# Kernel tuning notes

Hardware: AMD Instinct MI355X
Metric: run time of the kernel (lower is better)

## Reference

```python
import jax, jax.numpy as jnp
import numpy as np

B, S, D = 2, 4096, 2048
HQ, HK, HV = 32, 8, 8
H = max(HQ, HK, HV)
DK, DV = 64, 64
OUT = 2048
CHUNK = 64  # chunked-recurrent block size


def setup_inputs() -> dict:
    key = jax.random.key(0)
    k1, k2, k3 = jax.random.split(key, 3)
    x = jax.random.normal(k1, (B, S, D), dtype=jnp.float32)
    input_state = jnp.zeros((B, H * DK * DV), dtype=jnp.float32)
    qkv = HQ * DK + HK * DK + HV * DV  # 3072
    # Linear weights stored as [in, out]; equals torch weight.T so y = x @ W
    W_in = jax.random.normal(k2, (D, qkv), dtype=jnp.float32) * (D ** -0.5)
    W_out = jax.random.normal(k3, (H * DV, OUT), dtype=jnp.float32) * ((H * DV) ** -0.5)
    return {"x": x, "input_state": input_state, "W_in": W_in, "W_out": W_out}


def _linear_attention(q, k, v, S0):
    # q,k,v: [B,S,H,d]; S0: [B,H,DK,DV]
    nc = S // CHUNK
    # move chunk axis to front for lax.scan: [nc, B, CHUNK, H, d]
    qc = jnp.moveaxis(q.reshape(B, nc, CHUNK, H, DK), 1, 0)
    kc = jnp.moveaxis(k.reshape(B, nc, CHUNK, H, DK), 1, 0)
    vc = jnp.moveaxis(v.reshape(B, nc, CHUNK, H, DV), 1, 0)
    mask = jnp.tril(jnp.ones((CHUNK, CHUNK), dtype=bool))  # causal within chunk

    def step(Sstate, blk):
        qb, kb, vb = blk  # [B,C,H,d]
        A = jnp.einsum('bihd,bjhd->bhij', qb, kb)
        A = jnp.where(mask, A, jnp.zeros((), A.dtype))
        o = jnp.einsum('bhij,bjhd->bihd', A, vb) \
            + jnp.einsum('bihd,bhde->bihe', qb, Sstate)
        Sstate = Sstate + jnp.einsum('bjhd,bjhe->bhde', kb, vb)
        return Sstate, o

    Sf, o = jax.lax.scan(step, S0, (qc, kc, vc))
    o = jnp.moveaxis(o, 0, 1).reshape(B, S, H, DV)
    return o, Sf


def reference(x, input_state, W_in, W_out):
    proj = x @ W_in  # [B,S,3072]
    q, k, v = jnp.split(proj, [HQ * DK, HQ * DK + HK * DK], axis=-1)
    q = q.reshape(B, S, HQ, DK)
    k = k.reshape(B, S, HK, DK)
    v = v.reshape(B, S, HV, DV)
    # GQA: repeat kv heads up to num_heads = max(...)
    k = jnp.repeat(k, H // HK, axis=2)
    v = jnp.repeat(v, H // HV, axis=2)
    S0 = input_state.reshape(B, H, DK, DV)
    o, Sf = _linear_attention(q, k, v, S0)
    out = o.reshape(B, S, H * DV) @ W_out
    return out, Sf.reshape(B, H, DK * DV)
```

## Files before the change

### kernel.cpp

```cpp
#include <hip/hip_runtime.h>

typedef __bf16 bf16_t;
typedef __bf16 bf16x8 __attribute__((ext_vector_type(8)));
typedef __bf16 bf16x4 __attribute__((ext_vector_type(4)));
typedef float  f32x4  __attribute__((ext_vector_type(4)));

#define MFMA16(a,b,c) __builtin_amdgcn_mfma_f32_16x16x32_bf16((a),(b),(c),0,0,0)

__device__ __forceinline__ void gl_lds16(const void* g, void* l) {
    __builtin_amdgcn_global_load_lds(
        (__attribute__((address_space(1))) void*)(g),
        (__attribute__((address_space(3))) void*)(l),
        16, 0, 0);
}

static constexpr int S_TOT   = 8192;
static constexpr int D_IN    = 2048;
static constexpr int QKV     = 3072;
static constexpr int OUT_D   = 2048;
static constexpr int NCHUNK  = 64;
static constexpr int ZSTR    = 88;

__global__ __launch_bounds__(256)
void prep(const float* __restrict__ x, bf16_t* __restrict__ xb,
          const float* __restrict__ W_in, bf16_t* __restrict__ WinT,
          const float* __restrict__ W_out, bf16_t* __restrict__ WoutT) {
    __shared__ float tile[64][65];
    const int bid = blockIdx.x;
    const int t   = threadIdx.x;
    if (bid < 16384) {
        int i = bid * 256 + t;
        f32x4 v = ((const f32x4*)x)[i];
        bf16x4 o;
        o[0] = (bf16_t)v[0]; o[1] = (bf16_t)v[1]; o[2] = (bf16_t)v[2]; o[3] = (bf16_t)v[3];
        ((bf16x4*)xb)[i] = o;
        return;
    }
    const float* in; bf16_t* out; int R, C, bx, by;
    int tb = bid - 16384;
    if (tb < 1536) { in = W_in;  out = WinT;  R = 2048; C = 3072; bx = tb % 48; by = tb / 48; }
    else { tb -= 1536; in = W_out; out = WoutT; R = 2048; C = 2048; bx = tb % 32; by = tb / 32; }
    const int r0 = by * 64, c0 = bx * 64;
#pragma unroll
    for (int p = 0; p < 4; p++) {
        int row = p * 16 + (t >> 4);
        int col = (t & 15) * 4;
        f32x4 v = *(const f32x4*)&in[(size_t)(r0 + row) * C + c0 + col];
        tile[row][col + 0] = v[0]; tile[row][col + 1] = v[1];
        tile[row][col + 2] = v[2]; tile[row][col + 3] = v[3];
    }
    __syncthreads();
#pragma unroll
    for (int p = 0; p < 4; p++) {
        int oc  = p * 16 + (t >> 4);
        int orr = (t & 15) * 4;
        bf16x4 v;
        v[0] = (bf16_t)tile[orr + 0][oc]; v[1] = (bf16_t)tile[orr + 1][oc];
        v[2] = (bf16_t)tile[orr + 2][oc]; v[3] = (bf16_t)tile[orr + 3][oc];
        *(bf16x4*)&out[(size_t)(c0 + oc) * R + r0 + orr] = v;
    }
}

template<int OUT_BF16>
__global__ __launch_bounds__(256, 4)
void gemm_bt(const bf16_t* __restrict__ A, const bf16_t* __restrict__ Bt,
             void* __restrict__ Cout, int M, int N, int K) {
    __shared__ alignas(16) bf16_t lA[128 * 64];
    __shared__ alignas(16) bf16_t lB[128 * 64];
    const int tid = threadIdx.x;
    const int m0 = blockIdx.y * 128;
    const int n0 = blockIdx.x * 128;
    const int w = tid >> 6, lane = tid & 63;
    const int wr = (w >> 1) * 64, wc = (w & 1) * 64;
    const int l15 = lane & 15, q = lane >> 4, q4 = q * 4;
    const int trow = tid >> 3;
    const int tcc  = (tid & 7) ^ (trow & 7);
    const bf16_t* Ag = A + (size_t)(m0 + trow) * K + tcc * 8;
    const bf16_t* Bg = Bt + (size_t)(n0 + trow) * K + tcc * 8;
    bf16_t* lA_t = lA + tid * 8;
    bf16_t* lB_t = lB + tid * 8;
    const size_t rs = (size_t)32 * K;
    const int cc0 = (q)     ^ (l15 & 7);
    const int cc1 = (4 + q) ^ (l15 & 7);
    f32x4 acc[4][4] = {};
    for (int k0 = 0; k0 < K; k0 += 64) {
#pragma unroll
        for (int j = 0; j < 4; j++) {
            gl_lds16(Ag + k0 + j * rs, lA_t + j * 2048);
            gl_lds16(Bg + k0 + j * rs, lB_t + j * 2048);
        }
        __syncthreads();
#pragma unroll
        for (int ksub = 0; ksub < 2; ksub++) {
            const int cc = ksub ? cc1 : cc0;
            bf16x8 bfr[4];
#pragma unroll
            for (int nj = 0; nj < 4; nj++)
                bfr[nj] = *(const bf16x8*)&lB[(wc + nj * 16 + l15) * 64 + cc * 8];
#pragma unroll
            for (int mi = 0; mi < 4; mi++) {
                bf16x8 afr = *(const bf16x8*)&lA[(wr + mi * 16 + l15) * 64 + cc * 8];
#pragma unroll
                for (int nj = 0; nj < 4; nj++)
                    acc[mi][nj] = MFMA16(afr, bfr[nj], acc[mi][nj]);
            }
        }
        __syncthreads();
    }
    if (OUT_BF16) {
        bf16_t* C = (bf16_t*)Cout;
#pragma unroll
        for (int mi = 0; mi < 4; mi++)
#pragma unroll
            for (int nj = 0; nj < 4; nj++)
#pragma unroll
                for (int r = 0; r < 4; r++)
                    C[(size_t)(m0 + wr + mi * 16 + q4 + r) * N + n0 + wc + nj * 16 + l15] =
                        (bf16_t)acc[mi][nj][r];
    } else {
        float* C = (float*)Cout;
#pragma unroll
        for (int mi = 0; mi < 4; mi++)
#pragma unroll
            for (int nj = 0; nj < 4; nj++)
#pragma unroll
                for (int r = 0; r < 4; r++)
                    C[(size_t)(m0 + wr + mi * 16 + q4 + r) * N + n0 + wc + nj * 16 + l15] =
                        acc[mi][nj][r];
    }
}

__global__ __launch_bounds__(64)
void kv_fused(const bf16_t* __restrict__ proj, bf16_t* __restrict__ vT_g,
              float* __restrict__ Zc) {
    const int idx = blockIdx.x;
    const int c = idx & 63, hk = (idx >> 6) & 7, b = idx >> 9;
    const int tokBase = b * 4096 + c * 64;
    __shared__ float tk[64][65];
    __shared__ float tv[64][65];
    const int lane = threadIdx.x;
    const bf16_t* kg = proj + (size_t)tokBase * QKV + 2048 + hk * 64;
    const bf16_t* vg = proj + (size_t)tokBase * QKV + 2560 + hk * 64;
#pragma unroll
    for (int p = 0; p < 8; p++) {
        int tok = p * 8 + (lane >> 3);
        int d0  = (lane & 7) * 8;
        bf16x8 kv = *(const bf16x8*)&kg[(size_t)tok * QKV + d0];
        bf16x8 vv = *(const bf16x8*)&vg[(size_t)tok * QKV + d0];
#pragma unroll
        for (int e = 0; e < 8; e++) {
            tk[tok][d0 + e] = (float)kv[e];
            tv[tok][d0 + e] = (float)vv[e];
        }
    }
    __syncthreads();
#pragma unroll
    for (int p = 0; p < 8; p++) {
        int dv = p * 8 + (lane >> 3);
        int t0 = (lane & 7) * 8;
        bf16x8 o;
#pragma unroll
        for (int e = 0; e < 8; e++) o[e] = (bf16_t)tv[t0 + e][dv];
        *(bf16x8*)&vT_g[(size_t)idx * 4096 + dv * 64 + t0] = o;
    }
    const int l15 = lane & 15, q8 = (lane >> 4) * 8, q4 = (lane >> 4) * 4;
    f32x4 acc[4][4] = {};
#pragma unroll
    for (int ks = 0; ks < 2; ks++) {
        bf16x8 af[4], bf_[4];
#pragma unroll
        for (int mi = 0; mi < 4; mi++)
#pragma unroll
            for (int e = 0; e < 8; e++) af[mi][e] = (bf16_t)tv[ks * 32 + q8 + e][mi * 16 + l15];
#pragma unroll
        for (int nj = 0; nj < 4; nj++)
#pragma unroll
            for (int e = 0; e < 8; e++) bf_[nj][e] = (bf16_t)tk[ks * 32 + q8 + e][nj * 16 + l15];
#pragma unroll
        for (int mi = 0; mi < 4; mi++)
#pragma unroll
            for (int nj = 0; nj < 4; nj++)
                acc[mi][nj] = MFMA16(af[mi], bf_[nj], acc[mi][nj]);
    }
    float* zout = Zc + (size_t)idx * 4096;
#pragma unroll
    for (int mi = 0; mi < 4; mi++)
#pragma unroll
        for (int nj = 0; nj < 4; nj++)
#pragma unroll
            for (int r = 0; r < 4; r++)
                zout[(mi * 16 + q4 + r) * 64 + nj * 16 + l15] = acc[mi][nj][r];
}

__global__ __launch_bounds__(256)
void prefix_state(const float* __restrict__ Zc, const float* __restrict__ S0,
                  bf16_t* __restrict__ Zp, float* __restrict__ SfOut) {
    const int slice = blockIdx.x & 15;
    const int bh = blockIdx.x >> 4;
    const int h = bh & 31, b = bh >> 5;
    const int hk = h >> 2;
    const int e = slice * 256 + threadIdx.x;
    const int dv = e >> 6, dk = e & 63;
    float acc = S0[(size_t)b * 131072 + h * 4096 + dk * 64 + dv];
    const float* zc = Zc + ((size_t)(b * 8 + hk) * 64) * 4096 + e;
    bf16_t* zp = Zp + ((size_t)(b * 32 + h) * 64) * 4096 + e;
#pragma unroll 4
    for (int c = 0; c < NCHUNK; c++) {
        zp[(size_t)c * 4096] = (bf16_t)acc;
        acc += zc[(size_t)c * 4096];
    }
    SfOut[(size_t)b * 131072 + h * 4096 + dk * 64 + dv] = acc;
}

__global__ __launch_bounds__(256)
void attn_chunk(const bf16_t* __restrict__ proj, const bf16_t* __restrict__ vT_g,
                const bf16_t* __restrict__ Zp, bf16_t* __restrict__ O) {
    const int idx = blockIdx.x;
    const int hk = idx & 7, c = (idx >> 3) & 63, b = idx >> 9;
    const int g = threadIdx.x >> 6, lane = threadIdx.x & 63;
    const int h = hk * 4 + g;
    const int tokBase = b * 4096 + c * 64;
    __shared__ alignas(16) bf16_t zs_all[4][64 * ZSTR];
    bf16_t* zs = zs_all[g];
    const int l15 = lane & 15, q8 = (lane >> 4) * 8, q4 = (lane >> 4) * 4;
    const bf16_t* qrow  = proj + (size_t)tokBase * QKV + h * 64;
    const bf16_t* krow  = proj + (size_t)tokBase * QKV + 2048 + hk * 64;
    const bf16_t* zrow  = Zp + (((size_t)(b * 32 + h)) * 64 + c) * 4096;
    const bf16_t* vTrow = vT_g + ((size_t)(b * 8 + hk) * 64 + c) * 4096;

    bf16x8 qf[2][4];
#pragma unroll
    for (int ks = 0; ks < 2; ks++)
#pragma unroll
        for (int mi = 0; mi < 4; mi++)
            qf[ks][mi] = *(const bf16x8*)&qrow[(size_t)(mi * 16 + l15) * QKV + ks * 32 + q8];

    f32x4 oacc[4][4] = {};
#pragma unroll
    for (int ks = 0; ks < 2; ks++) {
        bf16x8 zf[4];
#pragma unroll
        for (int nj = 0; nj < 4; nj++) zf[nj] = *(const bf16x8*)&zrow[(nj * 16 + l15) * 64 + ks * 32 + q8];
#pragma unroll
        for (int mi = 0; mi < 4; mi++)
#pragma unroll
            for (int nj = 0; nj < 4; nj++)
                oacc[mi][nj] = MFMA16(qf[ks][mi], zf[nj], oacc[mi][nj]);
    }
    f32x4 sacc[4][4] = {};
#pragma unroll
    for (int ks = 0; ks < 2; ks++) {
        bf16x8 kf[4];
#pragma unroll
        for (int nj = 0; nj < 4; nj++) kf[nj] = *(const bf16x8*)&krow[(size_t)(nj * 16 + l15) * QKV + ks * 32 + q8];
#pragma unroll
        for (int mi = 0; mi < 4; mi++)
#pragma unroll
            for (int nj = 0; nj < 4; nj++)
                if (mi >= nj) sacc[mi][nj] = MFMA16(qf[ks][mi], kf[nj], sacc[mi][nj]);
    }
#pragma unroll
    for (int mi = 0; mi < 4; mi++)
#pragma unroll
        for (int nj = 0; nj < 4; nj++)
#pragma unroll
            for (int r = 0; r < 4; r++) {
                int ti = mi * 16 + q4 + r, tj = nj * 16 + l15;
                float v = (ti >= tj) ? sacc[mi][nj][r] : 0.0f;
                zs[ti * ZSTR + tj] = (bf16_t)v;
            }
    __syncthreads();
#pragma unroll
    for (int ks = 0; ks < 2; ks++) {
        bf16x8 sf[4], vf[4];
#pragma unroll
        for (int mi = 0; mi < 4; mi++) sf[mi] = *(const bf16x8*)&zs[(mi * 16 + l15) * ZSTR + ks * 32 + q8];
#pragma unroll
        for (int nj = 0; nj < 4; nj++) vf[nj] = *(const bf16x8*)&vTrow[(nj * 16 + l15) * 64 + ks * 32 + q8];
#pragma unroll
        for (int mi = 0; mi < 4; mi++)
#pragma unroll
            for (int nj = 0; nj < 4; nj++)
                oacc[mi][nj] = MFMA16(sf[mi], vf[nj], oacc[mi][nj]);
    }
    bf16_t* og = O + (size_t)tokBase * OUT_D + h * 64;
#pragma unroll
    for (int mi = 0; mi < 4; mi++)
#pragma unroll
        for (int nj = 0; nj < 4; nj++)
#pragma unroll
            for (int r = 0; r < 4; r++)
                og[(size_t)(mi * 16 + q4 + r) * OUT_D + nj * 16 + l15] = (bf16_t)oacc[mi][nj][r];
}

extern "C" void kernel_launch(void* const* d_in, const int* in_sizes, int n_in,
                              void* d_out, int out_size, void* d_ws, size_t ws_size,
                              hipStream_t stream) {
    const float* x     = (const float*)d_in[0];
    const float* S0    = (const float*)d_in[1];
    const float* W_in  = (const float*)d_in[2];
    const float* W_out = (const float*)d_in[3];

    char* ws = (char*)d_ws;
    bf16_t* xb    = (bf16_t*)(ws + 0);
    bf16_t* WinT  = (bf16_t*)(ws + 33554432);
    bf16_t* WoutT = (bf16_t*)(ws + 46137344);
    bf16_t* proj  = (bf16_t*)(ws + 54525952);
    float*  Zc    = (float*) (ws + 104857600);
    bf16_t* Zp    = (bf16_t*)(ws + 121634816);
    bf16_t* vT_g  = (bf16_t*)(ws + 0);
    bf16_t* Ob    = (bf16_t*)(ws + 8388608);

    float* outMain  = (float*)d_out;
    float* outState = (float*)d_out + (size_t)S_TOT * OUT_D;

    prep<<<16384 + 1536 + 1024, 256, 0, stream>>>(x, xb, W_in, WinT, W_out, WoutT);
    gemm_bt<1><<<dim3(24, 64), 256, 0, stream>>>(xb, WinT, proj, S_TOT, QKV, D_IN);
    kv_fused<<<1024, 64, 0, stream>>>(proj, vT_g, Zc);
    prefix_state<<<1024, 256, 0, stream>>>(Zc, S0, Zp, outState);
    attn_chunk<<<1024, 256, 0, stream>>>(proj, vT_g, Zp, Ob);
    gemm_bt<0><<<dim3(16, 64), 256, 0, stream>>>(Ob, WoutT, outMain, S_TOT, OUT_D, OUT_D);
}
```

Baseline: 369.2 us.

## Replace GEMM with triple-buffered 128x256 pipelined kernel and swizzled block order

Replaces the 128x128 single-buffered GEMM with a 128x256 tile kernel that uses triple-buffered LDS with K-step 32, issuing async global-to-LDS loads two tiles ahead and waiting with vmcnt, so memory latency overlaps the MFMA work. It also remaps block IDs in groups of 8 for better L2 locality and raises MFMA priority with setprio. Each wave now holds a 128x64 accumulator tile, which raises register pressure and lowers occupancy (launch bounds 2), and the grid becomes 1D with 768 and 512 workgroups.

```diff
diff --git a/kernel.cpp b/kernel.cpp
--- a/kernel.cpp
+++ b/kernel.cpp
@@ -62,70 +62,95 @@
 }
 
 template<int OUT_BF16>
-__global__ __launch_bounds__(256, 4)
-void gemm_bt(const bf16_t* __restrict__ A, const bf16_t* __restrict__ Bt,
-             void* __restrict__ Cout, int M, int N, int K) {
-    __shared__ alignas(16) bf16_t lA[128 * 64];
-    __shared__ alignas(16) bf16_t lB[128 * 64];
+__global__ __launch_bounds__(256, 2)
+void gemm_pipe(const bf16_t* __restrict__ A, const bf16_t* __restrict__ Bt,
+               void* __restrict__ Cout, int M, int N, int K) {
+    __shared__ alignas(16) bf16_t lA[3][128 * 32];
+    __shared__ alignas(16) bf16_t lB[3][256 * 32];
     const int tid = threadIdx.x;
-    const int m0 = blockIdx.y * 128;
-    const int n0 = blockIdx.x * 128;
+    const int nwg = gridDim.x;
+    int id = blockIdx.x;
+    id = (id & 7) * (nwg >> 3) + (id >> 3);
+    const int mt = M >> 7;
+    const int m0 = (id % mt) * 128;
+    const int n0 = (id / mt) * 256;
     const int w = tid >> 6, lane = tid & 63;
-    const int wr = (w >> 1) * 64, wc = (w & 1) * 64;
     const int l15 = lane & 15, q = lane >> 4, q4 = q * 4;
-    const int trow = tid >> 3;
-    const int tcc  = (tid & 7) ^ (trow & 7);
-    const bf16_t* Ag = A + (size_t)(m0 + trow) * K + tcc * 8;
-    const bf16_t* Bg = Bt + (size_t)(n0 + trow) * K + tcc * 8;
-    bf16_t* lA_t = lA + tid * 8;
-    bf16_t* lB_t = lB + tid * 8;
-    const size_t rs = (size_t)32 * K;
-    const int cc0 = (q)     ^ (l15 & 7);
-    const int cc1 = (4 + q) ^ (l15 & 7);
-    f32x4 acc[4][4] = {};
-    for (int k0 = 0; k0 < K; k0 += 64) {
-#pragma unroll
-        for (int j = 0; j < 4; j++) {
-            gl_lds16(Ag + k0 + j * rs, lA_t + j * 2048);
-            gl_lds16(Bg + k0 + j * rs, lB_t + j * 2048);
+    const int trow = tid >> 2;
+    const int scc  = (tid & 3) ^ (trow & 3);
+    const bf16_t* Ag = A  + (size_t)(m0 + trow) * K + scc * 8;
+    const bf16_t* Bg = Bt + (size_t)(n0 + trow) * K + scc * 8;
+    const size_t r64 = (size_t)64 * K;
+    const int rq   = q ^ (l15 & 3);
+    const int aoff = l15 * 32 + rq * 8;
+    const int boff = (w * 64 + l15) * 32 + rq * 8;
+    f32x4 acc[8][4] = {};
+    const int NT = K >> 5;
+#pragma unroll
+    for (int pt = 0; pt < 2; pt++) {
+        gl_lds16(Ag + pt * 32,       &lA[pt][tid * 8]);
+        gl_lds16(Ag + r64 + pt * 32, &lA[pt][2048 + tid * 8]);
+#pragma unroll
+        for (int i = 0; i < 4; i++)
+            gl_lds16(Bg + (size_t)i * r64 + pt * 32, &lB[pt][i * 2048 + tid * 8]);
+    }
+    asm volatile("s_waitcnt vmcnt(6)" ::: "memory");
+    __builtin_amdgcn_sched_barrier(0);
+    __builtin_amdgcn_s_barrier();
+    int buf = 0, sbuf = 2, kk = 64;
+    for (int t = 0; t < NT; t++) {
+        if (t + 2 < NT) {
+            gl_lds16(Ag + kk,       &lA[sbuf][tid * 8]);
+            gl_lds16(Ag + r64 + kk, &lA[sbuf][2048 + tid * 8]);
+#pragma unroll
+            for (int i = 0; i < 4; i++)
+                gl_lds16(Bg + (size_t)i * r64 + kk, &lB[sbuf][i * 2048 + tid * 8]);
         }
-        __syncthreads();
-#pragma unroll
-        for (int ksub = 0; ksub < 2; ksub++) {
-            const int cc = ksub ? cc1 : cc0;
-            bf16x8 bfr[4];
-#pragma unroll
-            for (int nj = 0; nj < 4; nj++)
-                bfr[nj] = *(const bf16x8*)&lB[(wc + nj * 16 + l15) * 64 + cc * 8];
-#pragma unroll
-            for (int mi = 0; mi < 4; mi++) {
-                bf16x8 afr = *(const bf16x8*)&lA[(wr + mi * 16 + l15) * 64 + cc * 8];
-#pragma unroll
-                for (int nj = 0; nj < 4; nj++)
-                    acc[mi][nj] = MFMA16(afr, bfr[nj], acc[mi][nj]);
-            }
+        bf16x8 afr[8], bfr[4];
+#pragma unroll
+        for (int nj = 0; nj < 4; nj++)
+            bfr[nj] = *(const bf16x8*)&lB[buf][boff + nj * 512];
+#pragma unroll
+        for (int mi = 0; mi < 8; mi++)
+            afr[mi] = *(const bf16x8*)&lA[buf][aoff + mi * 512];
+        __builtin_amdgcn_s_barrier();
+        __builtin_amdgcn_s_setprio(1);
+#pragma unroll
+        for (int mi = 0; mi < 8; mi++)
+#pragma unroll
+            for (int nj = 0; nj < 4; nj++)
+                acc[mi][nj] = MFMA16(afr[mi], bfr[nj], acc[mi][nj]);
+        __builtin_amdgcn_s_setprio(0);
+        if (t + 2 < NT) {
+            asm volatile("s_waitcnt vmcnt(6)" ::: "memory");
+        } else if (t + 1 < NT) {
+            asm volatile("s_waitcnt vmcnt(0)" ::: "memory");
         }
-        __syncthreads();
+        __builtin_amdgcn_sched_barrier(0);
+        __builtin_amdgcn_s_barrier();
+        kk += 32;
+        buf  = (buf  == 2) ? 0 : buf  + 1;
+        sbuf = (sbuf == 2) ? 0 : sbuf + 1;
     }
     if (OUT_BF16) {
         bf16_t* C = (bf16_t*)Cout;
 #pragma unroll
-        for (int mi = 0; mi < 4; mi++)
+        for (int mi = 0; mi < 8; mi++)
 #pragma unroll
             for (int nj = 0; nj < 4; nj++)
 #pragma unroll
                 for (int r = 0; r < 4; r++)
-                    C[(size_t)(m0 + wr + mi * 16 + q4 + r) * N + n0 + wc + nj * 16 + l15] =
+                    C[(size_t)(m0 + mi * 16 + q4 + r) * N + n0 + w * 64 + nj * 16 + l15] =
                         (bf16_t)acc[mi][nj][r];
     } else {
         float* C = (float*)Cout;
 #pragma unroll
-        for (int mi = 0; mi < 4; mi++)
+        for (int mi = 0; mi < 8; mi++)
 #pragma unroll
             for (int nj = 0; nj < 4; nj++)
 #pragma unroll
                 for (int r = 0; r < 4; r++)
-                    C[(size_t)(m0 + wr + mi * 16 + q4 + r) * N + n0 + wc + nj * 16 + l15] =
+                    C[(size_t)(m0 + mi * 16 + q4 + r) * N + n0 + w * 64 + nj * 16 + l15] =
                         acc[mi][nj][r];
     }
 }
@@ -315,9 +340,9 @@
     float* outState = (float*)d_out + (size_t)S_TOT * OUT_D;
 
     prep<<<16384 + 1536 + 1024, 256, 0, stream>>>(x, xb, W_in, WinT, W_out, WoutT);
-    gemm_bt<1><<<dim3(24, 64), 256, 0, stream>>>(xb, WinT, proj, S_TOT, QKV, D_IN);
+    gemm_pipe<1><<<768, 256, 0, stream>>>(xb, WinT, proj, S_TOT, QKV, D_IN);
     kv_fused<<<1024, 64, 0, stream>>>(proj, vT_g, Zc);
     prefix_state<<<1024, 256, 0, stream>>>(Zc, S0, Zp, outState);
     attn_chunk<<<1024, 256, 0, stream>>>(proj, vT_g, Zp, Ob);
-    gemm_bt<0><<<dim3(16, 64), 256, 0, stream>>>(Ob, WoutT, outMain, S_TOT, OUT_D, OUT_D);
-}
+    gemm_pipe<0><<<512, 256, 0, stream>>>(Ob, WoutT, outMain, S_TOT, OUT_D, OUT_D);
+}
```

Measured after the change: 422.2 us. +14.4%, slower.

## Replace GEMM with 256x256-tile double-buffered 8-wave pipelined kernel

Applied to the files above, without the earlier changes.

Replaces the 128x128 single-buffered GEMM with a 256x256 tile kernel using 512 threads, double-buffered LDS with global-to-LDS prefetch of the next K tile interleaved with MFMA work, fine-grained waitcnt/barrier scheduling and setprio. It also remaps workgroup IDs in an XCD-aware way so neighbouring tiles share caches. This aims to hide global load latency and raise operand reuse in both projection GEMMs. The cost is more LDS per block (128KB), fewer resident blocks, and a fragile hand-tuned schedule that relies on the grid size dividing by 8.

```diff
diff --git a/kernel.cpp b/kernel.cpp
--- a/kernel.cpp
+++ b/kernel.cpp
@@ -62,57 +62,118 @@
 }
 
 template<int OUT_BF16>
-__global__ __launch_bounds__(256, 4)
-void gemm_bt(const bf16_t* __restrict__ A, const bf16_t* __restrict__ Bt,
-             void* __restrict__ Cout, int M, int N, int K) {
-    __shared__ alignas(16) bf16_t lA[128 * 64];
-    __shared__ alignas(16) bf16_t lB[128 * 64];
+__global__ __launch_bounds__(512, 2)
+void gemm8p(const bf16_t* __restrict__ A, const bf16_t* __restrict__ Bt,
+            void* __restrict__ Cout, int M, int N, int K, int nt) {
+    __shared__ alignas(16) bf16_t lds[2][2][16384];
     const int tid = threadIdx.x;
-    const int m0 = blockIdx.y * 128;
-    const int n0 = blockIdx.x * 128;
+    const int nwg = gridDim.x;
+    int id = blockIdx.x;
+    id = (id & 7) * (nwg >> 3) + (id >> 3);
+    const int n0 = (id % nt) * 256;
+    const int m0 = (id / nt) * 256;
     const int w = tid >> 6, lane = tid & 63;
-    const int wr = (w >> 1) * 64, wc = (w & 1) * 64;
     const int l15 = lane & 15, q = lane >> 4, q4 = q * 4;
+    const int wr = (w >> 1) * 64;
+    const int wc = (w & 1) * 128;
     const int trow = tid >> 3;
     const int tcc  = (tid & 7) ^ (trow & 7);
-    const bf16_t* Ag = A + (size_t)(m0 + trow) * K + tcc * 8;
+    const bf16_t* Ag = A  + (size_t)(m0 + trow) * K + tcc * 8;
     const bf16_t* Bg = Bt + (size_t)(n0 + trow) * K + tcc * 8;
-    bf16_t* lA_t = lA + tid * 8;
-    bf16_t* lB_t = lB + tid * 8;
-    const size_t rs = (size_t)32 * K;
-    const int cc0 = (q)     ^ (l15 & 7);
-    const int cc1 = (4 + q) ^ (l15 & 7);
-    f32x4 acc[4][4] = {};
-    for (int k0 = 0; k0 < K; k0 += 64) {
+    const size_t rK = (size_t)64 * K;
+    int aoff[2], boff[2];
+#pragma unroll
+    for (int ks = 0; ks < 2; ks++) {
+        aoff[ks] = (wr + l15) * 64 + (((ks * 4 + q) ^ (l15 & 7)) * 8);
+        boff[ks] = (wc + l15) * 64 + (((ks * 4 + q) ^ (l15 & 7)) * 8);
+    }
+    f32x4 acc[4][8] = {};
+    const int NT = K >> 6;
+    {
+        bf16_t* dA = &lds[0][0][0];
+        bf16_t* dB = &lds[0][1][0];
+        gl_lds16(Ag,            &dA[tid * 8]);
+        gl_lds16(Ag + rK,       &dA[4096  + tid * 8]);
+        gl_lds16(Ag + 2 * rK,   &dA[8192  + tid * 8]);
+        gl_lds16(Ag + 3 * rK,   &dA[12288 + tid * 8]);
+        gl_lds16(Bg,            &dB[tid * 8]);
+        gl_lds16(Bg + 2 * rK,   &dB[8192  + tid * 8]);
+        gl_lds16(Bg + rK,       &dB[4096  + tid * 8]);
+        gl_lds16(Bg + 3 * rK,   &dB[12288 + tid * 8]);
+    }
+    asm volatile("s_waitcnt vmcnt(2)" ::: "memory");
+    __builtin_amdgcn_sched_barrier(0);
+    __builtin_amdgcn_s_barrier();
+    for (int t = 0; t < NT; t++) {
+        const bf16_t* cA = &lds[t & 1][0][0];
+        const bf16_t* cB = &lds[t & 1][1][0];
+        bf16_t* sA = &lds[(t + 1) & 1][0][0];
+        bf16_t* sB = &lds[(t + 1) & 1][1][0];
+        const size_t kk = (size_t)(t + 1) * 64;
+        const bool st = (t + 1 < NT);
+        bf16x8 af[4][2];
 #pragma unroll
         for (int j = 0; j < 4; j++) {
-            gl_lds16(Ag + k0 + j * rs, lA_t + j * 2048);
-            gl_lds16(Bg + k0 + j * rs, lB_t + j * 2048);
+            bf16x8 bfr[2][2];
+            if (j == 0) {
+#pragma unroll
+                for (int mi = 0; mi < 4; mi++)
+#pragma unroll
+                    for (int ks = 0; ks < 2; ks++)
+                        af[mi][ks] = *(const bf16x8*)&cA[aoff[ks] + mi * 1024];
+            }
+#pragma unroll
+            for (int nj = 0; nj < 2; nj++)
+#pragma unroll
+                for (int ks = 0; ks < 2; ks++)
+                    bfr[nj][ks] = *(const bf16x8*)&cB[boff[ks] + (2 * j + nj) * 1024];
+            if (st) {
+                if (j == 0) {
+                    gl_lds16(Ag + kk,            &sA[tid * 8]);
+                    gl_lds16(Ag + rK + kk,       &sA[4096  + tid * 8]);
+                } else if (j == 1) {
+                    gl_lds16(Ag + 2 * rK + kk,   &sA[8192  + tid * 8]);
+                    gl_lds16(Ag + 3 * rK + kk,   &sA[12288 + tid * 8]);
+                } else if (j == 2) {
+                    gl_lds16(Bg + kk,            &sB[tid * 8]);
+                    gl_lds16(Bg + 2 * rK + kk,   &sB[8192  + tid * 8]);
+                } else {
+                    gl_lds16(Bg + rK + kk,       &sB[4096  + tid * 8]);
+                    gl_lds16(Bg + 3 * rK + kk,   &sB[12288 + tid * 8]);
+                }
+            }
+            __builtin_amdgcn_sched_barrier(0);
+            __builtin_amdgcn_s_barrier();
+            asm volatile("s_waitcnt lgkmcnt(0)" ::: "memory");
+            __builtin_amdgcn_sched_barrier(0);
+            __builtin_amdgcn_s_setprio(1);
+#pragma unroll
+            for (int mi = 0; mi < 4; mi++)
+#pragma unroll
+                for (int nj = 0; nj < 2; nj++)
+#pragma unroll
+                    for (int ks = 0; ks < 2; ks++)
+                        acc[mi][2 * j + nj] = MFMA16(af[mi][ks], bfr[nj][ks], acc[mi][2 * j + nj]);
+            __builtin_amdgcn_s_setprio(0);
+            if (j == 1) {
+                if (st) asm volatile("s_waitcnt vmcnt(4)" ::: "memory");
+                else    asm volatile("s_waitcnt vmcnt(0)" ::: "memory");
+                __builtin_amdgcn_sched_barrier(0);
+            } else if (j == 3) {
+                if (st) {
+                    asm volatile("s_waitcnt vmcnt(2)" ::: "memory");
+                    __builtin_amdgcn_sched_barrier(0);
+                }
+            }
+            __builtin_amdgcn_s_barrier();
         }
-        __syncthreads();
-#pragma unroll
-        for (int ksub = 0; ksub < 2; ksub++) {
-            const int cc = ksub ? cc1 : cc0;
-            bf16x8 bfr[4];
-#pragma unroll
-            for (int nj = 0; nj < 4; nj++)
-                bfr[nj] = *(const bf16x8*)&lB[(wc + nj * 16 + l15) * 64 + cc * 8];
-#pragma unroll
-            for (int mi = 0; mi < 4; mi++) {
-                bf16x8 afr = *(const bf16x8*)&lA[(wr + mi * 16 + l15) * 64 + cc * 8];
-#pragma unroll
-                for (int nj = 0; nj < 4; nj++)
-                    acc[mi][nj] = MFMA16(afr, bfr[nj], acc[mi][nj]);
-            }
-        }
-        __syncthreads();
     }
     if (OUT_BF16) {
         bf16_t* C = (bf16_t*)Cout;
 #pragma unroll
         for (int mi = 0; mi < 4; mi++)
 #pragma unroll
-            for (int nj = 0; nj < 4; nj++)
+            for (int nj = 0; nj < 8; nj++)
 #pragma unroll
                 for (int r = 0; r < 4; r++)
                     C[(size_t)(m0 + wr + mi * 16 + q4 + r) * N + n0 + wc + nj * 16 + l15] =
@@ -122,7 +183,7 @@
 #pragma unroll
         for (int mi = 0; mi < 4; mi++)
 #pragma unroll
-            for (int nj = 0; nj < 4; nj++)
+            for (int nj = 0; nj < 8; nj++)
 #pragma unroll
                 for (int r = 0; r < 4; r++)
                     C[(size_t)(m0 + wr + mi * 16 + q4 + r) * N + n0 + wc + nj * 16 + l15] =
@@ -315,9 +376,9 @@
     float* outState = (float*)d_out + (size_t)S_TOT * OUT_D;
 
     prep<<<16384 + 1536 + 1024, 256, 0, stream>>>(x, xb, W_in, WinT, W_out, WoutT);
-    gemm_bt<1><<<dim3(24, 64), 256, 0, stream>>>(xb, WinT, proj, S_TOT, QKV, D_IN);
+    gemm8p<1><<<384, 512, 0, stream>>>(xb, WinT, proj, S_TOT, QKV, D_IN, 12);
     kv_fused<<<1024, 64, 0, stream>>>(proj, vT_g, Zc);
     prefix_state<<<1024, 256, 0, stream>>>(Zc, S0, Zp, outState);
     attn_chunk<<<1024, 256, 0, stream>>>(proj, vT_g, Zp, Ob);
-    gemm_bt<0><<<dim3(16, 64), 256, 0, stream>>>(Ob, WoutT, outMain, S_TOT, OUT_D, OUT_D);
-}
+    gemm8p<0><<<256, 512, 0, stream>>>(Ob, WoutT, outMain, S_TOT, OUT_D, OUT_D, 8);
+}
```

Measured after the change: 381.8 us. +3.4%, slower.

## Double-buffer GEMM LDS tiles with prefetch and remap workgroups across XCDs

Applied to the files above, without the earlier changes.

Rewrites the bf16 GEMM used for the input and output projections so it double-buffers the LDS tiles. The next K-slice is loaded while MFMAs run on the current one, and there is one barrier per iteration instead of two. It also moves to a 1D grid whose block IDs are remapped so that neighbouring tiles share a chiplet (XCD), and raises wave priority around the MFMA block. The LDS footprint doubles and launch bounds drop to 2 blocks per CU, which lowers occupancy.

```diff
diff --git a/kernel.cpp b/kernel.cpp
--- a/kernel.cpp
+++ b/kernel.cpp
@@ -62,50 +62,75 @@
 }
 
 template<int OUT_BF16>
-__global__ __launch_bounds__(256, 4)
-void gemm_bt(const bf16_t* __restrict__ A, const bf16_t* __restrict__ Bt,
-             void* __restrict__ Cout, int M, int N, int K) {
-    __shared__ alignas(16) bf16_t lA[128 * 64];
-    __shared__ alignas(16) bf16_t lB[128 * 64];
+__global__ __launch_bounds__(256, 2)
+void gemm_p2(const bf16_t* __restrict__ A, const bf16_t* __restrict__ Bt,
+             void* __restrict__ Cout, int M, int N, int K, int ntile) {
+    __shared__ alignas(16) bf16_t lds[2][2][8192];
     const int tid = threadIdx.x;
-    const int m0 = blockIdx.y * 128;
-    const int n0 = blockIdx.x * 128;
+    const int nwg = gridDim.x;
+    int id = blockIdx.x;
+    id = (id & 7) * (nwg >> 3) + (id >> 3);
+    const int n0 = (id % ntile) * 128;
+    const int m0 = (id / ntile) * 128;
     const int w = tid >> 6, lane = tid & 63;
+    const int l15 = lane & 15, q = lane >> 4, q4 = q * 4;
     const int wr = (w >> 1) * 64, wc = (w & 1) * 64;
-    const int l15 = lane & 15, q = lane >> 4, q4 = q * 4;
     const int trow = tid >> 3;
     const int tcc  = (tid & 7) ^ (trow & 7);
-    const bf16_t* Ag = A + (size_t)(m0 + trow) * K + tcc * 8;
+    const bf16_t* Ag = A  + (size_t)(m0 + trow) * K + tcc * 8;
     const bf16_t* Bg = Bt + (size_t)(n0 + trow) * K + tcc * 8;
-    bf16_t* lA_t = lA + tid * 8;
-    bf16_t* lB_t = lB + tid * 8;
-    const size_t rs = (size_t)32 * K;
-    const int cc0 = (q)     ^ (l15 & 7);
-    const int cc1 = (4 + q) ^ (l15 & 7);
+    const size_t r32 = (size_t)32 * K;
+    int cc[2];
+    cc[0] = (q ^ (l15 & 7)) * 8;
+    cc[1] = ((4 + q) ^ (l15 & 7)) * 8;
     f32x4 acc[4][4] = {};
-    for (int k0 = 0; k0 < K; k0 += 64) {
-#pragma unroll
-        for (int j = 0; j < 4; j++) {
-            gl_lds16(Ag + k0 + j * rs, lA_t + j * 2048);
-            gl_lds16(Bg + k0 + j * rs, lB_t + j * 2048);
-        }
-        __syncthreads();
-#pragma unroll
-        for (int ksub = 0; ksub < 2; ksub++) {
-            const int cc = ksub ? cc1 : cc0;
-            bf16x8 bfr[4];
-#pragma unroll
-            for (int nj = 0; nj < 4; nj++)
-                bfr[nj] = *(const bf16x8*)&lB[(wc + nj * 16 + l15) * 64 + cc * 8];
-#pragma unroll
-            for (int mi = 0; mi < 4; mi++) {
-                bf16x8 afr = *(const bf16x8*)&lA[(wr + mi * 16 + l15) * 64 + cc * 8];
-#pragma unroll
-                for (int nj = 0; nj < 4; nj++)
-                    acc[mi][nj] = MFMA16(afr, bfr[nj], acc[mi][nj]);
+    const int NT = K >> 6;
+#pragma unroll
+    for (int j = 0; j < 4; j++) {
+        gl_lds16(Ag + j * r32, &lds[0][0][j * 2048 + tid * 8]);
+        gl_lds16(Bg + j * r32, &lds[0][1][j * 2048 + tid * 8]);
+    }
+    asm volatile("s_waitcnt vmcnt(0)" ::: "memory");
+    __builtin_amdgcn_sched_barrier(0);
+    __builtin_amdgcn_s_barrier();
+    __builtin_amdgcn_sched_barrier(0);
+    for (int t = 0; t < NT; t++) {
+        const int cb = t & 1;
+        if (t + 1 < NT) {
+            const size_t kk = (size_t)(t + 1) * 64;
+#pragma unroll
+            for (int j = 0; j < 4; j++) {
+                gl_lds16(Ag + j * r32 + kk, &lds[cb ^ 1][0][j * 2048 + tid * 8]);
+                gl_lds16(Bg + j * r32 + kk, &lds[cb ^ 1][1][j * 2048 + tid * 8]);
             }
         }
-        __syncthreads();
+        bf16x8 af[4][2], bfr[4][2];
+#pragma unroll
+        for (int mi = 0; mi < 4; mi++)
+#pragma unroll
+            for (int ks = 0; ks < 2; ks++)
+                af[mi][ks] = *(const bf16x8*)&lds[cb][0][(wr + mi * 16 + l15) * 64 + cc[ks]];
+#pragma unroll
+        for (int nj = 0; nj < 4; nj++)
+#pragma unroll
+            for (int ks = 0; ks < 2; ks++)
+                bfr[nj][ks] = *(const bf16x8*)&lds[cb][1][(wc + nj * 16 + l15) * 64 + cc[ks]];
+        __builtin_amdgcn_s_setprio(1);
+#pragma unroll
+        for (int mi = 0; mi < 4; mi++)
+#pragma unroll
+            for (int nj = 0; nj < 4; nj++)
+#pragma unroll
+                for (int ks = 0; ks < 2; ks++)
+                    acc[mi][nj] = MFMA16(af[mi][ks], bfr[nj][ks], acc[mi][nj]);
+        __builtin_amdgcn_s_setprio(0);
+        if (t + 1 < NT) {
+            __builtin_amdgcn_sched_barrier(0);
+            asm volatile("s_waitcnt vmcnt(0)" ::: "memory");
+            __builtin_amdgcn_sched_barrier(0);
+            __builtin_amdgcn_s_barrier();
+            __builtin_amdgcn_sched_barrier(0);
+        }
     }
     if (OUT_BF16) {
         bf16_t* C = (bf16_t*)Cout;
@@ -315,9 +340,9 @@
     float* outState = (float*)d_out + (size_t)S_TOT * OUT_D;
 
     prep<<<16384 + 1536 + 1024, 256, 0, stream>>>(x, xb, W_in, WinT, W_out, WoutT);
-    gemm_bt<1><<<dim3(24, 64), 256, 0, stream>>>(xb, WinT, proj, S_TOT, QKV, D_IN);
+    gemm_p2<1><<<1536, 256, 0, stream>>>(xb, WinT, proj, S_TOT, QKV, D_IN, 24);
     kv_fused<<<1024, 64, 0, stream>>>(proj, vT_g, Zc);
     prefix_state<<<1024, 256, 0, stream>>>(Zc, S0, Zp, outState);
     attn_chunk<<<1024, 256, 0, stream>>>(proj, vT_g, Zp, Ob);
-    gemm_bt<0><<<dim3(16, 64), 256, 0, stream>>>(Ob, WoutT, outMain, S_TOT, OUT_D, OUT_D);
-}
+    gemm_p2<0><<<1024, 256, 0, stream>>>(Ob, WoutT, outMain, S_TOT, OUT_D, OUT_D, 16);
+}
```

Result: no change. 367.0 us (-0.6%).
